# Performance work log

Hardware: AMD Instinct MI355X
Metric: run time of the kernel (lower is better)

## Reference

```python
import jax, jax.numpy as jnp
import numpy as np

B = 64
HIST_LEN, PRED_HORIZON = 10, 10
H = W = 200
RES = 0.1
INIT_X_IDX, INIT_Y_IDX = 100.0, 160.0
FRONT_EDGE, BACK_EDGE = 3.89, 1.043
HALF_BOX = (FRONT_EDGE + BACK_EDGE) / 2.0
CENTER_SHIFT = HALF_BOX - BACK_EDGE          # mid-circle shift along box heading
FRONT_SHIFT = 2.0 * HALF_BOX - 2.0 * BACK_EDGE
EMBED, HIDDEN, CNN_OUT, CNN_CH = 64, 128, 1000, 32
SIGMA = 1.8
THETA = 0.0


def setup_inputs() -> dict:
    key = jax.random.key(0)
    ks = jax.random.split(key, 16)
    def rn(k, shape, scale=0.02):
        return jax.random.normal(k, shape, dtype=jnp.float32) * scale
    return {
        "img_feature": jax.random.normal(ks[0], (B, 12, H, W), dtype=jnp.float32),
        "hist_points": rn(ks[1], (B, HIST_LEN, 4), 1.0),
        "hist_points_step": rn(ks[2], (B, HIST_LEN, 4), 0.1),
        "ego_rendering_heading": jax.random.uniform(ks[3], (B, 1), dtype=jnp.float32, maxval=2.0 * np.pi),
        "comp_w": rn(ks[4], (3, 12, 3, 3)),
        "comp_b": jnp.zeros((3,), jnp.float32),
        "cnn_w": rn(ks[5], (CNN_CH, 3, 3, 3)),
        "cnn_b": jnp.zeros((CNN_CH,), jnp.float32),
        "cnn_fc_w": rn(ks[6], (CNN_OUT, CNN_CH)),
        "cnn_fc_b": jnp.zeros((CNN_OUT,), jnp.float32),
        "embed_w": rn(ks[7], (EMBED, 4)),
        "embed_b": jnp.zeros((EMBED,), jnp.float32),
        "h0": rn(ks[8], (1, HIDDEN)),
        "c0": rn(ks[9], (1, HIDDEN)),
        "w_ih": rn(ks[10], (4 * HIDDEN, EMBED)),
        "w_hh": rn(ks[11], (4 * HIDDEN, HIDDEN)),
        "b_ih": jnp.zeros((4 * HIDDEN,), jnp.float32),
        "b_hh": jnp.zeros((4 * HIDDEN,), jnp.float32),
        "out_w": rn(ks[12], (4, HIDDEN + CNN_OUT)),
        "out_b": jnp.zeros((4,), jnp.float32),
    }


def _conv(x, w, b, stride):
    y = jax.lax.conv_general_dilated(x, w, (stride, stride), 'SAME',
                                     dimension_numbers=('NCHW', 'OIHW', 'NCHW'))
    return y + b[None, :, None, None]


def _forward(img_feature, hist_points, hist_points_step, ego_rendering_heading,
             comp_w, comp_b, cnn_w, cnn_b, cnn_fc_w, cnn_fc_b,
             embed_w, embed_b, h0, c0, w_ih, w_hh, b_ih, b_hh, out_w, out_b):
    bsz = img_feature.shape[0]
    # CNN encoder: 12->3 compression conv, then backbone (stand-in for mobilenet_v2) -> 1000-dim
    z = _conv(img_feature, comp_w, comp_b, 1)
    z = jax.nn.relu(_conv(z, cnn_w, cnn_b, 2))
    z = z.mean(axis=(2, 3))                       # (B, CNN_CH) global avg pool
    img_emb = z @ cnn_fc_w.T + cnn_fc_b           # (B, 1000)

    def lstm_cell(e, h, c):                       # pytorch gate order i, f, g, o
        g = e @ w_ih.T + b_ih + h @ w_hh.T + b_hh
        i, f, gg, o = jnp.split(g, 4, axis=-1)
        c2 = jax.nn.sigmoid(f) * c + jax.nn.sigmoid(i) * jnp.tanh(gg)
        return jax.nn.sigmoid(o) * jnp.tanh(c2), c2

    def embed(step):
        return jax.nn.relu(step @ embed_w.T + embed_b)

    h = jnp.tile(h0, (bsz, 1))
    c = jnp.tile(c0, (bsz, 1))

    # warm up LSTM on history displacements (torch loop t = 1 .. HIST_LEN-1)
    def hist_step(carry, step_t):
        h, c = carry
        h, c = lstm_cell(embed(step_t), h, c)
        return (h, c), None
    (h, c), _ = jax.lax.scan(hist_step, (h, c),
                             jnp.swapaxes(hist_points_step[:, 1:HIST_LEN], 0, 1))

    def pred_step(carry, _):
        h, c, pose = carry
        step = jnp.concatenate([h, img_emb], axis=1) @ out_w.T + out_b
        pose = pose + step
        h, c = lstm_cell(embed(step), h, c)
        return (h, c, pose), pose
    _, poses = jax.lax.scan(pred_step, (h, c, hist_points[:, HIST_LEN - 1]),
                            None, length=PRED_HORIZON)
    pred_traj = jnp.swapaxes(poses, 0, 1)         # (B, T, 4) == torch pred_traj[:, 1:, :]

    # three-circle gaussian rasterization, vectorized over all timesteps
    ego = ego_rendering_heading.reshape(bsz)      # (B,)
    x, y, hd = pred_traj[..., 0], pred_traj[..., 1], pred_traj[..., 2]
    box_heading = -hd - ego[:, None]              # (B, T)
    ho = -(ego - np.pi / 2.0)                     # heading_offset, (B,)
    cos_ho, sin_ho = jnp.cos(ho)[:, None], jnp.sin(ho)[:, None]
    px = INIT_X_IDX + (x * cos_ho - y * sin_ho) / RES   # rear center in image idx
    py = INIT_Y_IDX - (x * sin_ho + y * cos_ho) / RES
    cos_bh, sin_bh = jnp.cos(box_heading), jnp.sin(box_heading)

    # idx_mesh built with meshgrid indexing='ij' over (W, H); image is square
    gx, gy = jnp.meshgrid(jnp.arange(W, dtype=jnp.float32),
                          jnp.arange(H, dtype=jnp.float32), indexing='ij')
    ct, st = np.cos(THETA), np.sin(THETA)
    ga = ct * ct / (2 * SIGMA ** 2) + st * st / (2 * SIGMA ** 2)
    gb = -np.sin(2 * THETA) / (4 * SIGMA ** 2) + np.sin(2 * THETA) / (4 * SIGMA ** 2)
    gc = st * st / (2 * SIGMA ** 2) + ct * ct / (2 * SIGMA ** 2)

    def gauss(shift):
        cx = px + shift / RES * cos_bh            # (B, T)
        cy = py - shift / RES * sin_bh
        dx = gx[None, None] - cx[..., None, None] # (B, T, H, W)
        dy = gy[None, None] - cy[..., None, None]
        return jnp.exp(-(ga * dx * dx + 2 * gb * dx * dy + gc * dy * dy))

    boxes = jnp.maximum(gauss(0.0), jnp.maximum(gauss(CENTER_SHIFT), gauss(FRONT_SHIFT)))
    pred_boxs = boxes[:, :, None]                 # (B, T, 1, H, W)
    return pred_traj, pred_boxs


def reference(img_feature, hist_points, hist_points_step, ego_rendering_heading,
              comp_w, comp_b, cnn_w, cnn_b, cnn_fc_w, cnn_fc_b,
              embed_w, embed_b, h0, c0, w_ih, w_hh, b_ih, b_hh, out_w, out_b):
    return _forward(img_feature, hist_points, hist_points_step, ego_rendering_heading,
                    comp_w, comp_b, cnn_w, cnn_b, cnn_fc_w, cnn_fc_b,
                    embed_w, embed_b, h0, c0, w_ih, w_hh, b_ih, b_hh, out_w, out_b)
```

## Files before the change

### kernel.cpp

```cpp
#include <hip/hip_runtime.h>
#include <math.h>

typedef _Float16 f16;
typedef f16 f16x2 __attribute__((ext_vector_type(2)));

__device__ __forceinline__ float dot2acc(f16x2 a, f16x2 b, float c){
#if __has_builtin(__builtin_amdgcn_fdot2)
  return __builtin_amdgcn_fdot2(a, b, c, false);
#else
  return c + (float)a[0]*(float)b[0] + (float)a[1]*(float)b[1];
#endif
}

__global__ __launch_bounds__(256) void k_conv1(const float* __restrict__ img,
    const float* __restrict__ cw, const float* __restrict__ cb,
    float* __restrict__ c1){
  int b = blockIdx.y, ty = blockIdx.x;
  int t = threadIdx.x, lane = t & 63, wv = t >> 6;
  int y0 = ty*10;
  int cg = t % 50, rt = t / 50;

  __shared__ __align__(16) float sbuf[2][2404];

  int goff[3]; bool gact[3];
  #pragma unroll
  for (int j=0;j<3;++j){
    int k = wv + 4*j;
    int e = k*64 + lane;
    gact[j] = (k < 10) && (e < 600);
    int r = e/50, c4 = e - 50*r;
    int gy = y0 - 1 + r; gy = gy < 0 ? 0 : (gy > 199 ? 199 : gy);
    goff[j] = gy*200 + c4*4;
  }
  const float* cbase0 = img + (size_t)b*480000;

  bool rok[4];
  #pragma unroll
  for (int rr=0; rr<4; ++rr){
    int gy = y0 + rt*2 - 1 + rr;
    rok[rr] = (unsigned)gy < 200u;
  }
  bool xl = (cg>0), xr = (cg<49);

  float acc[3][2][4];
  #pragma unroll
  for (int oc=0;oc<3;++oc){
    float bz = cb[oc];
    #pragma unroll
    for (int jj=0;jj<2;++jj)
      #pragma unroll
      for (int c=0;c<4;++c) acc[oc][jj][c] = bz;
  }

  auto STAGE = [&](int buf, int ci){
    const float* cp = cbase0 + ci*40000;
    #pragma unroll
    for (int j=0;j<3;++j){
      if (gact[j]){
        int k = wv + 4*j;
        const float* g = cp + goff[j];
#if __has_builtin(__builtin_amdgcn_global_load_lds)
        __builtin_amdgcn_global_load_lds(
            (const __attribute__((address_space(1))) void*)g,
            (__attribute__((address_space(3))) void*)&sbuf[buf][k*256], 16, 0, 0);
#else
        *(float4*)&sbuf[buf][(k*64 + lane)*4] = *(const float4*)g;
#endif
      }
    }
  };

  STAGE(0, 0);
  __syncthreads();
  for (int ci=0; ci<12; ++ci){
    int cur = ci & 1;
    if (ci < 11) STAGE(cur^1, ci+1);
    if (t < 250){
      float vr[4][6];
      #pragma unroll
      for (int rr=0; rr<4; ++rr){
        int lr = rt*2 + rr;
        const float* rp = &sbuf[cur][lr*200 + 4*cg];
        if (rok[rr]){
          float4 m = *(const float4*)rp;
          vr[rr][0] = xl ? rp[-1] : 0.f;
          vr[rr][1] = m.x; vr[rr][2] = m.y; vr[rr][3] = m.z; vr[rr][4] = m.w;
          vr[rr][5] = xr ? rp[4] : 0.f;
        } else {
          #pragma unroll
          for (int q=0;q<6;++q) vr[rr][q] = 0.f;
        }
      }
      #pragma unroll
      for (int oc=0;oc<3;++oc){
        const float* wp = cw + oc*108 + ci*9;
        float w00=wp[0], w01=wp[1], w02=wp[2],
              w10=wp[3], w11=wp[4], w12=wp[5],
              w20=wp[6], w21=wp[7], w22=wp[8];
        #pragma unroll
        for (int jj=0;jj<2;++jj){
          #pragma unroll
          for (int c=0;c<4;++c){
            float s = acc[oc][jj][c];
            s = fmaf(vr[jj+0][c+0], w00, s); s = fmaf(vr[jj+0][c+1], w01, s); s = fmaf(vr[jj+0][c+2], w02, s);
            s = fmaf(vr[jj+1][c+0], w10, s); s = fmaf(vr[jj+1][c+1], w11, s); s = fmaf(vr[jj+1][c+2], w12, s);
            s = fmaf(vr[jj+2][c+0], w20, s); s = fmaf(vr[jj+2][c+1], w21, s); s = fmaf(vr[jj+2][c+2], w22, s);
            acc[oc][jj][c] = s;
          }
        }
      }
    }
    __syncthreads();
  }

  if (t < 250){
    float* ob = c1 + (size_t)b*120000;
    int y = y0 + rt*2;
    #pragma unroll
    for (int oc=0;oc<3;++oc)
      #pragma unroll
      for (int jj=0;jj<2;++jj)
        *(float4*)(ob + oc*40000 + (y+jj)*200 + 4*cg) =
          make_float4(acc[oc][jj][0], acc[oc][jj][1], acc[oc][jj][2], acc[oc][jj][3]);
  }
}

__global__ __launch_bounds__(256) void k_conv2(const float* __restrict__ c1,
    const float* __restrict__ w2, const float* __restrict__ b2,
    float* __restrict__ part){
  int b = blockIdx.y, ty = blockIdx.x;
  int t = threadIdx.x;
  float acc[32];
  #pragma unroll
  for (int co=0;co<32;++co) acc[co]=0.f;
  if (t < 250){
    int oy  = ty*5 + t/50;
    int ox0 = (t%50)*2;
    const float* cbs = c1 + (size_t)b*120000;
    bool xl = (ox0>0);
    float vr[3][3][5];
    #pragma unroll
    for (int ci=0;ci<3;++ci){
      #pragma unroll
      for (int ky=0;ky<3;++ky){
        int iy = 2*oy + ky - 1;
        bool rok = (iy >= 0);
        const float* rp = cbs + ci*40000 + iy*200 + 2*ox0;
        float4 m = rok ? *(const float4*)rp : make_float4(0.f,0.f,0.f,0.f);
        vr[ci][ky][0] = (rok && xl) ? rp[-1] : 0.f;
        vr[ci][ky][1] = m.x; vr[ci][ky][2] = m.y; vr[ci][ky][3] = m.z; vr[ci][ky][4] = m.w;
      }
    }
    #pragma unroll
    for (int c=0;c<2;++c){
      #pragma unroll
      for (int co=0;co<32;++co){
        float s = b2[co];
        #pragma unroll
        for (int ci=0;ci<3;++ci)
          #pragma unroll
          for (int ky=0;ky<3;++ky)
            #pragma unroll
            for (int kx=0;kx<3;++kx)
              s = fmaf(vr[ci][ky][2*c+kx], w2[co*27+ci*9+ky*3+kx], s);
        acc[co] += fmaxf(s, 0.f);
      }
    }
  }
  int lane = t&63, wv = t>>6;
  __shared__ float wred[4][32];
  #pragma unroll
  for (int co=0;co<32;++co){
    float s = acc[co];
    #pragma unroll
    for (int off=32; off; off>>=1) s += __shfl_down(s, off, 64);
    if (lane==0) wred[wv][co] = s;
  }
  __syncthreads();
  if (t < 32){
    float s = wred[0][t]+wred[1][t]+wred[2][t]+wred[3][t];
    part[(b*20+ty)*32 + t] = s;
  }
}

__global__ __launch_bounds__(256) void k_lstm(
    const float* __restrict__ hist_pts, const float* __restrict__ hist_step,
    const float* __restrict__ emb_w, const float* __restrict__ emb_b,
    const float* __restrict__ h0, const float* __restrict__ c0,
    const float* __restrict__ w_ih, const float* __restrict__ w_hh,
    const float* __restrict__ b_ih, const float* __restrict__ b_hh,
    const float* __restrict__ out_w, const float* __restrict__ out_b,
    const float* __restrict__ part, const float* __restrict__ fcw,
    const float* __restrict__ fcb, float* __restrict__ traj){
  int b = blockIdx.x; int t = threadIdx.x; int lane = t&63, wv = t>>6;

  __shared__ float zfc[32];
  __shared__ float wredfc[4][4];
  if (t < 32){
    float s = 0.f;
    #pragma unroll
    for (int p=0;p<20;++p) s += part[(b*20+p)*32 + t];
    zfc[t] = s * (1.f/10000.f);
  }
  __syncthreads();
  {
    float cp0=0.f, cp1=0.f, cp2=0.f, cp3=0.f;
    for (int o = t; o < 1000; o += 256){
      float s = fcb[o];
      #pragma unroll
      for (int k=0;k<32;++k) s = fmaf(fcw[o*32+k], zfc[k], s);
      cp0 = fmaf(s, out_w[0*1128+128+o], cp0);
      cp1 = fmaf(s, out_w[1*1128+128+o], cp1);
      cp2 = fmaf(s, out_w[2*1128+128+o], cp2);
      cp3 = fmaf(s, out_w[3*1128+128+o], cp3);
    }
    #pragma unroll
    for (int off=32; off; off>>=1){
      cp0 += __shfl_down(cp0, off, 64);
      cp1 += __shfl_down(cp1, off, 64);
      cp2 += __shfl_down(cp2, off, 64);
      cp3 += __shfl_down(cp3, off, 64);
    }
    if (lane==0){ wredfc[wv][0]=cp0; wredfc[wv][1]=cp1; wredfc[wv][2]=cp2; wredfc[wv][3]=cp3; }
  }
  __syncthreads();
  float cst = 0.f;
  if (t < 4) cst = out_b[t] + wredfc[0][t]+wredfc[1][t]+wredfc[2][t]+wredfc[3][t];

  int u  = (t<128) ? t       : t-128;
  int j1 = (t<128) ? t       : 128+u;
  int j2 = (t<128) ? 256+t   : 384+u;

  f16x2 w1[96], w2[96];
  {
    const float2* r1 = (const float2*)(w_ih + j1*64);
    const float2* r2 = (const float2*)(w_ih + j2*64);
    #pragma unroll
    for (int p=0;p<32;++p){
      float2 a = r1[p], c = r2[p];
      w1[p] = f16x2{(f16)a.x, (f16)a.y};
      w2[p] = f16x2{(f16)c.x, (f16)c.y};
    }
    const float2* q1 = (const float2*)(w_hh + j1*128);
    const float2* q2 = (const float2*)(w_hh + j2*128);
    #pragma unroll
    for (int p=0;p<64;++p){
      float2 a = q1[p], c = q2[p];
      w1[32+p] = f16x2{(f16)a.x, (f16)a.y};
      w2[32+p] = f16x2{(f16)c.x, (f16)c.y};
    }
  }
  float bias1 = b_ih[j1] + b_hh[j1];
  float bias2 = b_ih[j2] + b_hh[j2];

  __shared__ f16x2 xl[96];
  __shared__ float e_lds[64], h_lds[128], a_lds[128];
  __shared__ float step_lds[4], wred4[4];

  float c_reg = (t>=128) ? c0[u] : 0.f;
  if (t < 128) h_lds[t] = h0[t];

  auto cell = [&](){
    __syncthreads();
    if (t < 32)      xl[t]    = f16x2{(f16)e_lds[2*t],        (f16)e_lds[2*t+1]};
    else if (t < 96){ int p=t-32; xl[t] = f16x2{(f16)h_lds[2*p], (f16)h_lds[2*p+1]}; }
    __syncthreads();
    float acc1 = bias1, acc2 = bias2;
    #pragma unroll
    for (int cc=0; cc<12; ++cc){
      f16x2 xv[8];
      #pragma unroll
      for (int q=0;q<8;++q) xv[q] = xl[cc*8+q];
      #pragma unroll
      for (int q=0;q<8;++q){
        acc1 = dot2acc(w1[cc*8+q], xv[q], acc1);
        acc2 = dot2acc(w2[cc*8+q], xv[q], acc2);
      }
    }
    if (t < 128){
      float ig = 1.f/(1.f+expf(-acc1));
      float gg = tanhf(acc2);
      a_lds[t] = ig*gg;
    }
    __syncthreads();
    if (t >= 128){
      float ff = 1.f/(1.f+expf(-acc1));
      float oo = 1.f/(1.f+expf(-acc2));
      c_reg = ff*c_reg + a_lds[u];
      h_lds[u] = oo * tanhf(c_reg);
    }
  };

  for (int s=1; s<10; ++s){
    if (t < 64){
      const float* hp = hist_step + (size_t)(b*10+s)*4;
      float e = emb_b[t]
              + emb_w[t*4+0]*hp[0] + emb_w[t*4+1]*hp[1]
              + emb_w[t*4+2]*hp[2] + emb_w[t*4+3]*hp[3];
      e_lds[t] = fmaxf(e, 0.f);
    }
    cell();
  }

  float pose = (t<4) ? hist_pts[(size_t)(b*10+9)*4 + t] : 0.f;
  for (int it=0; it<10; ++it){
    __syncthreads();
    {
      const float* owr = out_w + wv*1128;
      float p_ = owr[2*lane]*h_lds[2*lane] + owr[2*lane+1]*h_lds[2*lane+1];
      #pragma unroll
      for (int off=32; off; off>>=1) p_ += __shfl_down(p_, off, 64);
      if (lane==0) wred4[wv] = p_;
    }
    __syncthreads();
    if (t < 4){
      float st = wred4[t] + cst;
      pose += st;
      traj[(size_t)(b*10+it)*4 + t] = pose;
      step_lds[t] = st;
    }
    __syncthreads();
    if (it < 9){
      if (t < 64){
        float e = emb_b[t]
                + emb_w[t*4+0]*step_lds[0] + emb_w[t*4+1]*step_lds[1]
                + emb_w[t*4+2]*step_lds[2] + emb_w[t*4+3]*step_lds[3];
        e_lds[t] = fmaxf(e, 0.f);
      }
      cell();
    }
  }
}

__global__ __launch_bounds__(256) void k_raster(const float* __restrict__ traj,
    const float* __restrict__ ego, float* __restrict__ boxes){
  int img = blockIdx.y;
  int b = img / 10;
  __shared__ float ctr[6];
  if (threadIdx.x == 0){
    float x  = traj[img*4+0];
    float y  = traj[img*4+1];
    float hd = traj[img*4+2];
    float eg = ego[b];
    float ho = 1.5707963267948966f - eg;
    float sho, cho; __sincosf(ho, &sho, &cho);
    float pxc = 100.f + (x*cho - y*sho)*10.f;
    float pyc = 160.f - (x*sho + y*cho)*10.f;
    float bh  = -hd - eg;
    float sbh, cbh; __sincosf(bh, &sbh, &cbh);
    const float CSH = 14.235f;
    const float FSH = 28.47f;
    ctr[0] = pxc;             ctr[1] = pyc;
    ctr[2] = pxc + CSH*cbh;   ctr[3] = pyc - CSH*sbh;
    ctr[4] = pxc + FSH*cbh;   ctr[5] = pyc - FSH*sbh;
  }
  __syncthreads();
  int f4 = blockIdx.x*256 + threadIdx.x;
  if (f4 >= 10000) return;
  int p0 = f4*4;
  int i = p0 / 200;
  int j = p0 % 200;
  float fi = (float)i, fj = (float)j;
  float c0x=ctr[0], c0y=ctr[1], c1x=ctr[2], c1y=ctr[3], c2x=ctr[4], c2y=ctr[5];
  float dx0 = fi-c0x, dx1 = fi-c1x, dx2 = fi-c2x;
  float A0 = dx0*dx0, A1 = dx1*dx1, A2 = dx2*dx2;
  const float GA = 0.15432098765432098f;
  float r[4];
  #pragma unroll
  for (int l=0;l<4;++l){
    float dj = fj + (float)l;
    float dy0 = dj-c0y, dy1 = dj-c1y, dy2 = dj-c2y;
    float d0 = fmaf(dy0,dy0,A0);
    float d1 = fmaf(dy1,dy1,A1);
    float d2 = fmaf(dy2,dy2,A2);
    float m = fminf(d0, fminf(d1,d2));
    r[l] = __expf(-m*GA);
  }
  *(float4*)(boxes + (size_t)img*40000 + p0) = make_float4(r[0],r[1],r[2],r[3]);
}

extern "C" void kernel_launch(void* const* d_in, const int* in_sizes, int n_in,
                              void* d_out, int out_size, void* d_ws, size_t ws_size,
                              hipStream_t stream) {
  (void)in_sizes; (void)n_in; (void)d_ws; (void)ws_size; (void)out_size;
  const float* img = (const float*)d_in[0];
  const float* hp  = (const float*)d_in[1];
  const float* hps = (const float*)d_in[2];
  const float* ego = (const float*)d_in[3];
  const float* cw  = (const float*)d_in[4];
  const float* cb  = (const float*)d_in[5];
  const float* c2w = (const float*)d_in[6];
  const float* c2b = (const float*)d_in[7];
  const float* fcw = (const float*)d_in[8];
  const float* fcb = (const float*)d_in[9];
  const float* ew  = (const float*)d_in[10];
  const float* eb  = (const float*)d_in[11];
  const float* h0  = (const float*)d_in[12];
  const float* c0  = (const float*)d_in[13];
  const float* wih = (const float*)d_in[14];
  const float* whh = (const float*)d_in[15];
  const float* bih = (const float*)d_in[16];
  const float* bhh = (const float*)d_in[17];
  const float* ow  = (const float*)d_in[18];
  const float* ob  = (const float*)d_in[19];

  float* out  = (float*)d_out;
  float* traj = out;
  float* S    = out + 2560;
  float* part = S;
  float* c1   = S + 50000;

  hipLaunchKernelGGL(k_conv1, dim3(20, 64), dim3(256), 0, stream, img, cw, cb, c1);
  hipLaunchKernelGGL(k_conv2, dim3(20, 64), dim3(256), 0, stream, c1, c2w, c2b, part);
  hipLaunchKernelGGL(k_lstm,  dim3(64),     dim3(256), 0, stream,
                     hp, hps, ew, eb, h0, c0, wih, whh, bih, bhh, ow, ob, part, fcw, fcb, traj);
  hipLaunchKernelGGL(k_raster, dim3(40, 640), dim3(256), 0, stream, traj, ego, S);
}
```

Measured before the change: 133.1 us.

## Fuse compression conv and stride-2 backbone conv into one kernel via LDS

Merges the 12->3 compression convolution and the stride-2 32-channel convolution into a single kernel. Each block computes 11 rows of the intermediate (including a halo row), stores them as fp16 in shared memory, and runs the second conv plus ReLU/pooling reduction from there. This removes the global round trip of the intermediate tensor and one kernel launch. In exchange it recomputes one halo row per tile, uses more LDS, and rounds the intermediate to half precision.

```diff
diff --git a/kernel.cpp b/kernel.cpp
--- a/kernel.cpp
+++ b/kernel.cpp
@@ -3,6 +3,7 @@
 
 typedef _Float16 f16;
 typedef f16 f16x2 __attribute__((ext_vector_type(2)));
+typedef f16 f16x4 __attribute__((ext_vector_type(4)));
 
 __device__ __forceinline__ float dot2acc(f16x2 a, f16x2 b, float c){
 #if __has_builtin(__builtin_amdgcn_fdot2)
@@ -12,45 +13,51 @@
 #endif
 }
 
-__global__ __launch_bounds__(256) void k_conv1(const float* __restrict__ img,
-    const float* __restrict__ cw, const float* __restrict__ cb,
-    float* __restrict__ c1){
+__global__ __launch_bounds__(256) void k_conv12(
+    const float* __restrict__ img, const float* __restrict__ cw, const float* __restrict__ cb,
+    const float* __restrict__ w2, const float* __restrict__ b2,
+    float* __restrict__ part){
   int b = blockIdx.y, ty = blockIdx.x;
   int t = threadIdx.x, lane = t & 63, wv = t >> 6;
   int y0 = ty*10;
-  int cg = t % 50, rt = t / 50;
-
-  __shared__ __align__(16) float sbuf[2][2404];
+
+  __shared__ __align__(16) float sbuf[2][2608];
+  __shared__ f16 zl_[3][2200];
+  __shared__ float wred[4][32];
 
   int goff[3]; bool gact[3];
   #pragma unroll
   for (int j=0;j<3;++j){
     int k = wv + 4*j;
     int e = k*64 + lane;
-    gact[j] = (k < 10) && (e < 600);
-    int r = e/50, c4 = e - 50*r;
-    int gy = y0 - 1 + r; gy = gy < 0 ? 0 : (gy > 199 ? 199 : gy);
+    gact[j] = (k < 11) && (e < 650);
+    int lr = e/50, c4 = e - 50*lr;
+    int gy = y0 - 2 + lr; gy = gy < 0 ? 0 : (gy > 199 ? 199 : gy);
     goff[j] = gy*200 + c4*4;
   }
   const float* cbase0 = img + (size_t)b*480000;
 
-  bool rok[4];
-  #pragma unroll
-  for (int rr=0; rr<4; ++rr){
-    int gy = y0 + rt*2 - 1 + rr;
-    rok[rr] = (unsigned)gy < 200u;
+  int cg = t % 50, rt = t / 50;
+  int base = (rt==0) ? 0 : 2*rt+1;
+  int NR   = (rt==0) ? 5 : 4;
+  int NS   = (rt==0) ? 3 : 2;
+  bool rok[5];
+  #pragma unroll
+  for (int rr=0; rr<5; ++rr){
+    int gy = y0 - 2 + base + rr;
+    rok[rr] = (rr < NR) && ((unsigned)gy < 200u);
   }
   bool xl = (cg>0), xr = (cg<49);
 
-  float acc[3][2][4];
-  #pragma unroll
-  for (int oc=0;oc<3;++oc){
-    float bz = cb[oc];
-    #pragma unroll
-    for (int jj=0;jj<2;++jj)
-      #pragma unroll
-      for (int c=0;c<4;++c) acc[oc][jj][c] = bz;
-  }
+  float acc[3][3][4];
+  #pragma unroll
+  for (int s=0;s<3;++s)
+    #pragma unroll
+    for (int oc=0;oc<3;++oc){
+      float bz = cb[oc];
+      #pragma unroll
+      for (int c=0;c<4;++c) acc[s][oc][c] = bz;
+    }
 
   auto STAGE = [&](int buf, int ci){
     const float* cp = cbase0 + ci*40000;
@@ -76,36 +83,38 @@
     int cur = ci & 1;
     if (ci < 11) STAGE(cur^1, ci+1);
     if (t < 250){
-      float vr[4][6];
-      #pragma unroll
-      for (int rr=0; rr<4; ++rr){
-        int lr = rt*2 + rr;
-        const float* rp = &sbuf[cur][lr*200 + 4*cg];
-        if (rok[rr]){
-          float4 m = *(const float4*)rp;
-          vr[rr][0] = xl ? rp[-1] : 0.f;
-          vr[rr][1] = m.x; vr[rr][2] = m.y; vr[rr][3] = m.z; vr[rr][4] = m.w;
-          vr[rr][5] = xr ? rp[4] : 0.f;
-        } else {
-          #pragma unroll
-          for (int q=0;q<6;++q) vr[rr][q] = 0.f;
+      float vr[5][6];
+      #pragma unroll
+      for (int rr=0; rr<5; ++rr){
+        if (rr < NR){
+          const float* rp = &sbuf[cur][(base+rr)*200 + 4*cg];
+          if (rok[rr]){
+            float4 m = *(const float4*)rp;
+            vr[rr][0] = xl ? rp[-1] : 0.f;
+            vr[rr][1] = m.x; vr[rr][2] = m.y; vr[rr][3] = m.z; vr[rr][4] = m.w;
+            vr[rr][5] = xr ? rp[4] : 0.f;
+          } else {
+            #pragma unroll
+            for (int q=0;q<6;++q) vr[rr][q] = 0.f;
+          }
         }
       }
       #pragma unroll
-      for (int oc=0;oc<3;++oc){
-        const float* wp = cw + oc*108 + ci*9;
-        float w00=wp[0], w01=wp[1], w02=wp[2],
-              w10=wp[3], w11=wp[4], w12=wp[5],
-              w20=wp[6], w21=wp[7], w22=wp[8];
+      for (int s=0; s<3; ++s){
+        if (s >= NS) break;
         #pragma unroll
-        for (int jj=0;jj<2;++jj){
+        for (int oc=0;oc<3;++oc){
+          const float* wp = cw + oc*108 + ci*9;
+          float w00=wp[0], w01=wp[1], w02=wp[2],
+                w10=wp[3], w11=wp[4], w12=wp[5],
+                w20=wp[6], w21=wp[7], w22=wp[8];
           #pragma unroll
           for (int c=0;c<4;++c){
-            float s = acc[oc][jj][c];
-            s = fmaf(vr[jj+0][c+0], w00, s); s = fmaf(vr[jj+0][c+1], w01, s); s = fmaf(vr[jj+0][c+2], w02, s);
-            s = fmaf(vr[jj+1][c+0], w10, s); s = fmaf(vr[jj+1][c+1], w11, s); s = fmaf(vr[jj+1][c+2], w12, s);
-            s = fmaf(vr[jj+2][c+0], w20, s); s = fmaf(vr[jj+2][c+1], w21, s); s = fmaf(vr[jj+2][c+2], w22, s);
-            acc[oc][jj][c] = s;
+            float ss = acc[s][oc][c];
+            ss = fmaf(vr[s+0][c+0], w00, ss); ss = fmaf(vr[s+0][c+1], w01, ss); ss = fmaf(vr[s+0][c+2], w02, ss);
+            ss = fmaf(vr[s+1][c+0], w10, ss); ss = fmaf(vr[s+1][c+1], w11, ss); ss = fmaf(vr[s+1][c+2], w12, ss);
+            ss = fmaf(vr[s+2][c+0], w20, ss); ss = fmaf(vr[s+2][c+1], w21, ss); ss = fmaf(vr[s+2][c+2], w22, ss);
+            acc[s][oc][c] = ss;
           }
         }
       }
@@ -114,64 +123,54 @@
   }
 
   if (t < 250){
-    float* ob = c1 + (size_t)b*120000;
-    int y = y0 + rt*2;
-    #pragma unroll
-    for (int oc=0;oc<3;++oc)
-      #pragma unroll
-      for (int jj=0;jj<2;++jj)
-        *(float4*)(ob + oc*40000 + (y+jj)*200 + 4*cg) =
-          make_float4(acc[oc][jj][0], acc[oc][jj][1], acc[oc][jj][2], acc[oc][jj][3]);
-  }
-}
-
-__global__ __launch_bounds__(256) void k_conv2(const float* __restrict__ c1,
-    const float* __restrict__ w2, const float* __restrict__ b2,
-    float* __restrict__ part){
-  int b = blockIdx.y, ty = blockIdx.x;
-  int t = threadIdx.x;
-  float acc[32];
-  #pragma unroll
-  for (int co=0;co<32;++co) acc[co]=0.f;
+    #pragma unroll
+    for (int s=0; s<3; ++s){
+      if (s >= NS) break;
+      int zl = base + s;
+      bool zero = (ty==0) && (zl==0);
+      #pragma unroll
+      for (int oc=0;oc<3;++oc){
+        f16x4 w4;
+        #pragma unroll
+        for (int c=0;c<4;++c) w4[c] = zero ? (f16)0.f : (f16)acc[s][oc][c];
+        *(f16x4*)&zl_[oc][zl*200 + 4*cg] = w4;
+      }
+    }
+  }
+  __syncthreads();
+
+  float a2[32];
+  #pragma unroll
+  for (int co=0;co<32;++co) a2[co]=0.f;
   if (t < 250){
-    int oy  = ty*5 + t/50;
-    int ox0 = (t%50)*2;
-    const float* cbs = c1 + (size_t)b*120000;
-    bool xl = (ox0>0);
-    float vr[3][3][5];
-    #pragma unroll
-    for (int ci=0;ci<3;++ci){
-      #pragma unroll
-      for (int ky=0;ky<3;++ky){
-        int iy = 2*oy + ky - 1;
-        bool rok = (iy >= 0);
-        const float* rp = cbs + ci*40000 + iy*200 + 2*ox0;
-        float4 m = rok ? *(const float4*)rp : make_float4(0.f,0.f,0.f,0.f);
-        vr[ci][ky][0] = (rok && xl) ? rp[-1] : 0.f;
-        vr[ci][ky][1] = m.x; vr[ci][ky][2] = m.y; vr[ci][ky][3] = m.z; vr[ci][ky][4] = m.w;
-      }
-    }
-    #pragma unroll
-    for (int c=0;c<2;++c){
+    #pragma unroll
+    for (int e=0;e<2;++e){
+      int u = t + 250*e;
+      int oyl = u/100, ox = u - 100*oyl;
+      float vtap[27]; int idx=0;
+      #pragma unroll
+      for (int ci2=0;ci2<3;++ci2)
+        #pragma unroll
+        for (int ky=0;ky<3;++ky){
+          int zr = 2*oyl + ky;
+          #pragma unroll
+          for (int kx=0;kx<3;++kx){
+            int zx = 2*ox + kx - 1;
+            vtap[idx++] = (zx >= 0) ? (float)zl_[ci2][zr*200 + zx] : 0.f;
+          }
+        }
       #pragma unroll
       for (int co=0;co<32;++co){
         float s = b2[co];
         #pragma unroll
-        for (int ci=0;ci<3;++ci)
-          #pragma unroll
-          for (int ky=0;ky<3;++ky)
-            #pragma unroll
-            for (int kx=0;kx<3;++kx)
-              s = fmaf(vr[ci][ky][2*c+kx], w2[co*27+ci*9+ky*3+kx], s);
-        acc[co] += fmaxf(s, 0.f);
-      }
-    }
-  }
-  int lane = t&63, wv = t>>6;
-  __shared__ float wred[4][32];
+        for (int q=0;q<27;++q) s = fmaf(vtap[q], w2[co*27+q], s);
+        a2[co] += fmaxf(s, 0.f);
+      }
+    }
+  }
   #pragma unroll
   for (int co=0;co<32;++co){
-    float s = acc[co];
+    float s = a2[co];
     #pragma unroll
     for (int off=32; off; off>>=1) s += __shfl_down(s, off, 64);
     if (lane==0) wred[wv][co] = s;
@@ -408,10 +407,9 @@
   float* traj = out;
   float* S    = out + 2560;
   float* part = S;
-  float* c1   = S + 50000;
-
-  hipLaunchKernelGGL(k_conv1, dim3(20, 64), dim3(256), 0, stream, img, cw, cb, c1);
-  hipLaunchKernelGGL(k_conv2, dim3(20, 64), dim3(256), 0, stream, c1, c2w, c2b, part);
+
+  hipLaunchKernelGGL(k_conv12, dim3(20, 64), dim3(256), 0, stream,
+                     img, cw, cb, c2w, c2b, part);
   hipLaunchKernelGGL(k_lstm,  dim3(64),     dim3(256), 0, stream,
                      hp, hps, ew, eb, h0, c0, wih, whh, bih, bhh, ow, ob, part, fcw, fcb, traj);
   hipLaunchKernelGGL(k_raster, dim3(40, 640), dim3(256), 0, stream, traj, ego, S);
```

Result: slower. 152.8 us (+14.8%).

## Store conv1 output in fp16 and halve conv1 row tile to double blocks

Applied to the files above, without the earlier changes.

The conv1 intermediate is now written as fp16 instead of fp32, which halves the global traffic between conv1 and conv2. conv2 reads it with f16x4 loads and converts to float. conv1 tiles also shrink from 10 rows to 5 rows per block, so the grid doubles to 40x64, each thread computes one row, and less LDS is used. The trade-offs are rounding error in the intermediate activations and more halo rows loaded relative to useful output.

```diff
diff --git a/kernel.cpp b/kernel.cpp
--- a/kernel.cpp
+++ b/kernel.cpp
@@ -3,6 +3,7 @@
 
 typedef _Float16 f16;
 typedef f16 f16x2 __attribute__((ext_vector_type(2)));
+typedef f16 f16x4 __attribute__((ext_vector_type(4)));
 
 __device__ __forceinline__ float dot2acc(f16x2 a, f16x2 b, float c){
 #if __has_builtin(__builtin_amdgcn_fdot2)
@@ -14,48 +15,44 @@
 
 __global__ __launch_bounds__(256) void k_conv1(const float* __restrict__ img,
     const float* __restrict__ cw, const float* __restrict__ cb,
-    float* __restrict__ c1){
+    f16* __restrict__ c1h){
   int b = blockIdx.y, ty = blockIdx.x;
   int t = threadIdx.x, lane = t & 63, wv = t >> 6;
-  int y0 = ty*10;
-  int cg = t % 50, rt = t / 50;
-
-  __shared__ __align__(16) float sbuf[2][2404];
-
-  int goff[3]; bool gact[3];
-  #pragma unroll
-  for (int j=0;j<3;++j){
+  int y0 = ty*5;
+
+  __shared__ __align__(16) float sbuf[2][1404];
+
+  int goff[2]; bool gact[2];
+  #pragma unroll
+  for (int j=0;j<2;++j){
     int k = wv + 4*j;
     int e = k*64 + lane;
-    gact[j] = (k < 10) && (e < 600);
-    int r = e/50, c4 = e - 50*r;
-    int gy = y0 - 1 + r; gy = gy < 0 ? 0 : (gy > 199 ? 199 : gy);
+    gact[j] = (e < 350);
+    int lr = e/50, c4 = e - 50*lr;
+    int gy = y0 - 1 + lr; gy = gy < 0 ? 0 : (gy > 199 ? 199 : gy);
     goff[j] = gy*200 + c4*4;
   }
   const float* cbase0 = img + (size_t)b*480000;
 
-  bool rok[4];
-  #pragma unroll
-  for (int rr=0; rr<4; ++rr){
-    int gy = y0 + rt*2 - 1 + rr;
-    rok[rr] = (unsigned)gy < 200u;
-  }
+  int cg = t % 50, r = t / 50;
+  int y = y0 + r;
+  bool rok[3];
+  #pragma unroll
+  for (int rr=0; rr<3; ++rr) rok[rr] = (unsigned)(y-1+rr) < 200u;
   bool xl = (cg>0), xr = (cg<49);
 
-  float acc[3][2][4];
+  float acc[3][4];
   #pragma unroll
   for (int oc=0;oc<3;++oc){
     float bz = cb[oc];
     #pragma unroll
-    for (int jj=0;jj<2;++jj)
-      #pragma unroll
-      for (int c=0;c<4;++c) acc[oc][jj][c] = bz;
+    for (int c=0;c<4;++c) acc[oc][c] = bz;
   }
 
   auto STAGE = [&](int buf, int ci){
     const float* cp = cbase0 + ci*40000;
     #pragma unroll
-    for (int j=0;j<3;++j){
+    for (int j=0;j<2;++j){
       if (gact[j]){
         int k = wv + 4*j;
         const float* g = cp + goff[j];
@@ -76,11 +73,10 @@
     int cur = ci & 1;
     if (ci < 11) STAGE(cur^1, ci+1);
     if (t < 250){
-      float vr[4][6];
-      #pragma unroll
-      for (int rr=0; rr<4; ++rr){
-        int lr = rt*2 + rr;
-        const float* rp = &sbuf[cur][lr*200 + 4*cg];
+      float vr[3][6];
+      #pragma unroll
+      for (int rr=0; rr<3; ++rr){
+        const float* rp = &sbuf[cur][(r+rr)*200 + 4*cg];
         if (rok[rr]){
           float4 m = *(const float4*)rp;
           vr[rr][0] = xl ? rp[-1] : 0.f;
@@ -98,15 +94,12 @@
               w10=wp[3], w11=wp[4], w12=wp[5],
               w20=wp[6], w21=wp[7], w22=wp[8];
         #pragma unroll
-        for (int jj=0;jj<2;++jj){
-          #pragma unroll
-          for (int c=0;c<4;++c){
-            float s = acc[oc][jj][c];
-            s = fmaf(vr[jj+0][c+0], w00, s); s = fmaf(vr[jj+0][c+1], w01, s); s = fmaf(vr[jj+0][c+2], w02, s);
-            s = fmaf(vr[jj+1][c+0], w10, s); s = fmaf(vr[jj+1][c+1], w11, s); s = fmaf(vr[jj+1][c+2], w12, s);
-            s = fmaf(vr[jj+2][c+0], w20, s); s = fmaf(vr[jj+2][c+1], w21, s); s = fmaf(vr[jj+2][c+2], w22, s);
-            acc[oc][jj][c] = s;
-          }
+        for (int c=0;c<4;++c){
+          float s = acc[oc][c];
+          s = fmaf(vr[0][c+0], w00, s); s = fmaf(vr[0][c+1], w01, s); s = fmaf(vr[0][c+2], w02, s);
+          s = fmaf(vr[1][c+0], w10, s); s = fmaf(vr[1][c+1], w11, s); s = fmaf(vr[1][c+2], w12, s);
+          s = fmaf(vr[2][c+0], w20, s); s = fmaf(vr[2][c+1], w21, s); s = fmaf(vr[2][c+2], w22, s);
+          acc[oc][c] = s;
         }
       }
     }
@@ -114,18 +107,18 @@
   }
 
   if (t < 250){
-    float* ob = c1 + (size_t)b*120000;
-    int y = y0 + rt*2;
-    #pragma unroll
-    for (int oc=0;oc<3;++oc)
-      #pragma unroll
-      for (int jj=0;jj<2;++jj)
-        *(float4*)(ob + oc*40000 + (y+jj)*200 + 4*cg) =
-          make_float4(acc[oc][jj][0], acc[oc][jj][1], acc[oc][jj][2], acc[oc][jj][3]);
-  }
-}
-
-__global__ __launch_bounds__(256) void k_conv2(const float* __restrict__ c1,
+    f16* ob = c1h + (size_t)b*120000;
+    #pragma unroll
+    for (int oc=0;oc<3;++oc){
+      f16x4 w4;
+      #pragma unroll
+      for (int c=0;c<4;++c) w4[c] = (f16)acc[oc][c];
+      *(f16x4*)(ob + oc*40000 + y*200 + 4*cg) = w4;
+    }
+  }
+}
+
+__global__ __launch_bounds__(256) void k_conv2(const f16* __restrict__ c1h,
     const float* __restrict__ w2, const float* __restrict__ b2,
     float* __restrict__ part){
   int b = blockIdx.y, ty = blockIdx.x;
@@ -134,10 +127,10 @@
   #pragma unroll
   for (int co=0;co<32;++co) acc[co]=0.f;
   if (t < 250){
-    int oy  = ty*5 + t/50;
-    int ox0 = (t%50)*2;
-    const float* cbs = c1 + (size_t)b*120000;
-    bool xl = (ox0>0);
+    int oy = ty*5 + t/50;
+    int g  = t % 50;
+    const f16* cbs = c1h + (size_t)b*120000;
+    bool xl = (g>0);
     float vr[3][3][5];
     #pragma unroll
     for (int ci=0;ci<3;++ci){
@@ -145,10 +138,16 @@
       for (int ky=0;ky<3;++ky){
         int iy = 2*oy + ky - 1;
         bool rok = (iy >= 0);
-        const float* rp = cbs + ci*40000 + iy*200 + 2*ox0;
-        float4 m = rok ? *(const float4*)rp : make_float4(0.f,0.f,0.f,0.f);
-        vr[ci][ky][0] = (rok && xl) ? rp[-1] : 0.f;
-        vr[ci][ky][1] = m.x; vr[ci][ky][2] = m.y; vr[ci][ky][3] = m.z; vr[ci][ky][4] = m.w;
+        const f16* rp = cbs + ci*40000 + iy*200 + 4*g;
+        if (rok){
+          f16x4 m = *(const f16x4*)rp;
+          vr[ci][ky][0] = xl ? (float)rp[-1] : 0.f;
+          vr[ci][ky][1] = (float)m[0]; vr[ci][ky][2] = (float)m[1];
+          vr[ci][ky][3] = (float)m[2]; vr[ci][ky][4] = (float)m[3];
+        } else {
+          #pragma unroll
+          for (int q=0;q<5;++q) vr[ci][ky][q] = 0.f;
+        }
       }
     }
     #pragma unroll
@@ -408,10 +407,10 @@
   float* traj = out;
   float* S    = out + 2560;
   float* part = S;
-  float* c1   = S + 50000;
-
-  hipLaunchKernelGGL(k_conv1, dim3(20, 64), dim3(256), 0, stream, img, cw, cb, c1);
-  hipLaunchKernelGGL(k_conv2, dim3(20, 64), dim3(256), 0, stream, c1, c2w, c2b, part);
+  f16*   c1h  = (f16*)(S + 50000);
+
+  hipLaunchKernelGGL(k_conv1, dim3(40, 64), dim3(256), 0, stream, img, cw, cb, c1h);
+  hipLaunchKernelGGL(k_conv2, dim3(20, 64), dim3(256), 0, stream, c1h, c2w, c2b, part);
   hipLaunchKernelGGL(k_lstm,  dim3(64),     dim3(256), 0, stream,
                      hp, hps, ew, eb, h0, c0, wih, whh, bih, bhh, ow, ob, part, fcw, fcb, traj);
   hipLaunchKernelGGL(k_raster, dim3(40, 640), dim3(256), 0, stream, traj, ego, S);
```

After: 135.4 us. Within noise of the previous version (+1.8%).
